# Optimization experiments

Hardware: AMD Instinct MI355X
Metric: run time of the kernel (lower is better)

The kernel has to match this reference:

```python
import jax, jax.numpy as jnp
import numpy as np


def setup_inputs() -> dict:
    key = jax.random.key(0)
    k1, k2, k3 = jax.random.split(key, 3)
    B, N, D = 4, 4096, 256
    val = jax.random.normal(k1, (B, N, D), dtype=jnp.float32)
    state = jax.random.normal(k2, (B, N), dtype=jnp.float32)
    # val projection weight, scaled for unit-variance outputs
    Wv = jax.random.normal(k3, (D, D), dtype=jnp.float32) / np.sqrt(D)
    return {"val": val, "state": state, "Wv": Wv}


def reference(val, state, Wv):
    # pairwise_fn: dot-product scores over all node pairs -> [B, N, N]
    scores = jnp.einsum("bnd,bmd->bnm", val, val)
    # edge_compress_fn: softsign (non-softmax elementwise nonlinearity)
    edges = scores / (1.0 + jnp.abs(scores))
    # state_proj_fn = identity, val_proj_fn = linear
    projected_state = state                                  # [B, N]
    projected_val = jnp.einsum("bmd,de->bme", val, Wv)       # [B, N, D]
    # dual aggregation reusing the same edge matrix
    delta_state = jnp.einsum("bnm,bm->bn", edges, projected_state)
    delta_val = jnp.einsum("bnm,bmd->bnd", edges, projected_val)
    return (delta_state, delta_val)
```

## Files before the change

### kernel.cpp

```cpp
#include <hip/hip_runtime.h>

typedef unsigned short u16;
typedef unsigned char u8;
typedef unsigned int u32;
typedef __bf16 bf16x8 __attribute__((ext_vector_type(8)));
typedef float  f32x16 __attribute__((ext_vector_type(16)));
typedef int    i32x4  __attribute__((ext_vector_type(4)));
typedef int    i32x16 __attribute__((ext_vector_type(16)));

#define NB 4
#define NN 4096
#define ND 256

#define QPV (127.0f / 4.5f)
#define DPV (4.5f / 16129.0f)
#define QST (127.0f / 4.6f)
#define DST (4.6f / 16129.0f)
#define MAGIC 12582912.0f

__device__ __forceinline__ u16 f2bf(float x) { return __builtin_bit_cast(u16, (__bf16)x); }
__device__ __forceinline__ u32 fbits(float x) { return __builtin_bit_cast(u32, x); }

__device__ __forceinline__ u32 packlow4(float a, float b, float c, float d) {
    u32 p = __builtin_amdgcn_perm(fbits(b), fbits(a), 0x00000400u);
    u32 q = __builtin_amdgcn_perm(fbits(d), fbits(c), 0x00000400u);
    return __builtin_amdgcn_perm(q, p, 0x05040100u);
}

typedef __attribute__((address_space(1))) const u32 gas_u32;
typedef __attribute__((address_space(3))) u32 las_u32;
__device__ __forceinline__ void async_ld16(void* lds, const void* g) {
    __builtin_amdgcn_global_load_lds((gas_u32*)g, (las_u32*)lds, 16, 0, 0);
}


__global__ __launch_bounds__(256) void k_prep(const float* __restrict__ val,
                                              const float* __restrict__ state,
                                              const float* __restrict__ Wv,
                                              u16* __restrict__ kq, u8* __restrict__ kq8,
                                              float* __restrict__ srow,
                                              u8* __restrict__ vp8, u16* __restrict__ wv) {
    int tid = threadIdx.x;
    int bid = blockIdx.x;
    if (bid < 512) {
        __shared__ float t[32 * 257];
        __shared__ float rmax[32];
        const float* src = val + (size_t)bid * 32 * 256;
        #pragma unroll
        for (int k = 0; k < 8; k++) {
            int idx = tid + k * 256;
            int row = idx >> 6, c4 = idx & 63;
            float4 v = *(const float4*)(src + row * 256 + c4 * 4);
            float* p = t + row * 257 + c4 * 4;
            p[0] = v.x; p[1] = v.y; p[2] = v.z; p[3] = v.w;
        }
        __syncthreads();
        {
            int row = tid >> 3, seg = tid & 7;
            float m = 0.0f;
            #pragma unroll
            for (int i = 0; i < 32; i++) m = fmaxf(m, fabsf(t[row * 257 + seg + i * 8]));
            m = fmaxf(m, __shfl_down(m, 4));
            m = fmaxf(m, __shfl_down(m, 2));
            m = fmaxf(m, __shfl_down(m, 1));
            if (seg == 0) {
                m = fmaxf(m, 1e-20f);
                rmax[row] = m;
                srow[bid * 32 + row] = m * (1.0f / 127.0f);
            }
        }
        __syncthreads();
        u16* dst = kq + (size_t)bid * 16 * 512;
        #pragma unroll
        for (int k = 0; k < 4; k++) {
            int flat = tid + k * 256;
            int s = flat >> 6, l = flat & 63;
            int l31 = l & 31, h = l >> 5;
            const float* p = t + l31 * 257 + s * 16 + h * 8;
            union { u16 o[8]; uint4 q; } u;
            #pragma unroll
            for (int j = 0; j < 8; j++) u.o[j] = f2bf(p[j]);
            *(uint4*)(dst + (size_t)flat * 8) = u.q;
        }
        u8* dst8 = kq8 + (size_t)bid * 8192;
        #pragma unroll
        for (int k = 0; k < 2; k++) {
            int flat = tid + k * 256;
            int s = flat >> 6, l = flat & 63;
            int l31 = l & 31, h = l >> 5;
            float r127 = 127.0f / rmax[l31];
            const float* p = t + l31 * 257 + s * 32 + h * 16;
            u32 d[4];
            #pragma unroll
            for (int g = 0; g < 4; g++)
                d[g] = packlow4(fmaf(p[4 * g + 0], r127, MAGIC), fmaf(p[4 * g + 1], r127, MAGIC),
                                fmaf(p[4 * g + 2], r127, MAGIC), fmaf(p[4 * g + 3], r127, MAGIC));
            *(uint4*)(dst8 + (size_t)flat * 16) = make_uint4(d[0], d[1], d[2], d[3]);
        }
    } else if (bid < 516) {
        int b = bid - 512;
        __shared__ u8 qs[4096];
        #pragma unroll
        for (int k = 0; k < 16; k++) {
            int i = tid + k * 256;
            float x = fminf(fmaxf(state[b * 4096 + i] * QST, -127.0f), 127.0f);
            qs[i] = (u8)(fbits(x + MAGIC) & 255);
        }
        __syncthreads();
        #pragma unroll
        for (int k = 0; k < 32; k++) {
            int chunk = tid + k * 256;
            int strip = chunk >> 6, lane = chunk & 63, h = (lane >> 5) & 1;
            i32x4 v = *(const i32x4*)(qs + strip * 32 + h * 16);
            *(i32x4*)(vp8 + ((size_t)((b * 128 + strip) * 9 + 8)) * 1024 + (chunk & 63) * 16) = v;
        }
    } else {
        __shared__ u16 t2[256 * 33];
        int es = bid - 516, e0 = es * 32;
        #pragma unroll
        for (int k = 0; k < 8; k++) {
            int idx = tid + k * 256;
            int row = idx >> 3, c4 = idx & 7;
            float4 v = *(const float4*)(Wv + row * 256 + e0 + c4 * 4);
            u16* p = t2 + row * 33 + c4 * 4;
            p[0] = f2bf(v.x); p[1] = f2bf(v.y); p[2] = f2bf(v.z); p[3] = f2bf(v.w);
        }
        __syncthreads();
        u16* dst = wv + (size_t)es * 16 * 512;
        #pragma unroll
        for (int k = 0; k < 4; k++) {
            int flat = tid + k * 256;
            int s = flat >> 6, l = flat & 63;
            int l31 = l & 31, h = l >> 5;
            union { u16 o[8]; uint4 q; } u;
            #pragma unroll
            for (int j = 0; j < 8; j++) u.o[j] = t2[(s * 16 + h * 8 + j) * 33 + l31];
            *(uint4*)(dst + (size_t)flat * 8) = u.q;
        }
    }
}

__global__ __launch_bounds__(256) void k_pv(const u16* __restrict__ kq, const u16* __restrict__ wv,
                                            u8* __restrict__ vp8) {
    __shared__ u8 tp[4][32 * 48];
    int tid = threadIdx.x;
    int w = tid >> 6, lane = tid & 63;
    int l31 = lane & 31, h = lane >> 5;
    int wid = blockIdx.x * 4 + w;
    int bb = wid >> 8, es = (wid >> 5) & 7, qb = wid & 31;
    const u16* wvb = wv + (size_t)(es * 16) * 512 + lane * 8;
    const u16* kqb = kq + ((size_t)(bb * 128 + qb * 4) * 16) * 512 + lane * 8;
    f32x16 acc[4] = {};
    for (int s = 0; s < 16; s++) {
        bf16x8 af = *(const bf16x8*)(wvb + s * 512);
        #pragma unroll
        for (int qt = 0; qt < 4; qt++) {
            bf16x8 bfr = *(const bf16x8*)(kqb + (size_t)(qt * 16 + s) * 512);
            acc[qt] = __builtin_amdgcn_mfma_f32_32x32x16_bf16(af, bfr, acc[qt], 0, 0, 0);
        }
    }
    u8* myp = tp[w];
    #pragma unroll
    for (int qt = 0; qt < 4; qt++) {
        #pragma unroll
        for (int r = 0; r < 16; r++) {
            int erow = (r & 3) + 8 * (r >> 2) + 4 * h;
            float x = fminf(fmaxf(acc[qt][r] * QPV, -127.0f), 127.0f);
            myp[erow * 48 + l31] = (u8)(fbits(x + MAGIC) & 255);
        }
        i32x4 v = *(const i32x4*)(myp + l31 * 48 + h * 16);
        *(i32x4*)(vp8 + ((size_t)((bb * 128 + qb * 4 + qt) * 9 + es)) * 1024 + lane * 16) = v;
    }
}

__device__ __forceinline__ void stage_wave(u8* dst, const u8* src, int lane) {
    #pragma unroll
    for (int k = 0; k < 9; k++) {
        int c = lane + k * 64;
        async_ld16(dst + (size_t)c * 16, src + (size_t)c * 16);
    }
}

__global__ __launch_bounds__(256, 2) void k_main(const u8* __restrict__ kq8,
                                                 const u8* __restrict__ vp8,
                                                 const float* __restrict__ srow,
                                                 float* __restrict__ ds_out,
                                                 float* __restrict__ dval_out) {
    __shared__ u8 stage[2][4][9216];
    __shared__ int dsqi[4][32];

    int tid = threadIdx.x;
    int mq = tid >> 6, lane = tid & 63;
    int l31 = lane & 31, h = lane >> 5;

    int id = blockIdx.x;
    int xcd = id & 7;
    int bb = xcd >> 1;
    int t7 = ((xcd & 1) << 6) | (id >> 3);
    int q0 = t7 * 32;
    size_t bbase = (size_t)bb * 128;

    i32x4 qf[8];
    {
        const u8* qsrc = kq8 + (bbase + t7) * 8192 + lane * 16;
        #pragma unroll
        for (int s = 0; s < 8; s++) qf[s] = *(const i32x4*)(qsrc + (size_t)s * 1024);
    }
    float srq = srow[bb * 4096 + q0 + l31];

    i32x16 oacc[8] = {};
    i32x16 dsa = {};

    stage_wave(stage[0][mq], vp8 + (bbase + mq) * 9216, lane);

    for (int mt = 0; mt < 32; mt++) {
        const u8* kb = kq8 + (bbase + mt * 4 + mq) * 8192 + lane * 16;
        i32x4 kf[8];
        #pragma unroll
        for (int s = 0; s < 8; s++) kf[s] = *(const i32x4*)(kb + (size_t)s * 1024);
        const float* srm = srow + bb * 4096 + mt * 128 + mq * 32;
        float4 sg[4];
        #pragma unroll
        for (int g = 0; g < 4; g++) sg[g] = *(const float4*)(srm + g * 8 + h * 4);
        if (mt + 1 < 32)
            stage_wave(stage[(mt + 1) & 1][mq], vp8 + (bbase + (mt + 1) * 4 + mq) * 9216, lane);

        i32x16 sacc = {};
        #pragma unroll
        for (int s = 0; s < 8; s++)
            sacc = __builtin_amdgcn_mfma_i32_32x32x32_i8(kf[s], qf[s], sacc, 0, 0, 0);

        float cf[16];
        #pragma unroll
        for (int r = 0; r < 16; r++) {
            float sm = ((const float*)&sg[r >> 2])[r & 3] * srq;
            float xs = (float)sacc[r] * sm;
            float p = xs * __builtin_amdgcn_rcpf(1.0f + fabsf(xs));
            cf[r] = fmaf(p, 127.0f, MAGIC);
        }
        u32 w0 = packlow4(cf[0], cf[1], cf[2], cf[3]);
        u32 w1 = packlow4(cf[4], cf[5], cf[6], cf[7]);
        u32 w2 = packlow4(cf[8], cf[9], cf[10], cf[11]);
        u32 w3 = packlow4(cf[12], cf[13], cf[14], cf[15]);
        u32 x0 = (u32)__shfl_xor((int)w0, 32);
        u32 x1 = (u32)__shfl_xor((int)w1, 32);
        u32 x2 = (u32)__shfl_xor((int)w2, 32);
        u32 x3 = (u32)__shfl_xor((int)w3, 32);
        union { u32 wd[4]; i32x4 v; } pu;
        if (h == 0) { pu.wd[0] = w0; pu.wd[1] = x0; pu.wd[2] = w1; pu.wd[3] = x1; }
        else        { pu.wd[0] = x2; pu.wd[1] = w2; pu.wd[2] = x3; pu.wd[3] = w3; }
        i32x4 pf = pu.v;

        const u8* vb = stage[mt & 1][mq];
        #pragma unroll
        for (int et = 0; et < 8; et++) {
            i32x4 vf = *(const i32x4*)(vb + et * 1024 + lane * 16);
            oacc[et] = __builtin_amdgcn_mfma_i32_32x32x32_i8(pf, vf, oacc[et], 0, 0, 0);
        }
        {
            i32x4 sf = *(const i32x4*)(vb + 8 * 1024 + lane * 16);
            dsa = __builtin_amdgcn_mfma_i32_32x32x32_i8(pf, sf, dsa, 0, 0, 0);
        }
    }

    __syncthreads();

    if (l31 == 0) {
        #pragma unroll
        for (int r = 0; r < 16; r++) dsqi[mq][(r & 3) + 8 * (r >> 2) + 4 * h] = dsa[r];
    }
    int* red = (int*)stage;
    if (mq == 3) {
        #pragma unroll
        for (int et = 0; et < 8; et++)
            #pragma unroll
            for (int r = 0; r < 16; r++) {
                int row = (r & 3) + 8 * (r >> 2) + 4 * h;
                red[row * 256 + et * 32 + l31] = oacc[et][r];
            }
    }
    __syncthreads();
    if (mq == 2) {
        #pragma unroll
        for (int et = 0; et < 8; et++)
            #pragma unroll
            for (int r = 0; r < 16; r++) {
                int row = (r & 3) + 8 * (r >> 2) + 4 * h;
                red[row * 256 + et * 32 + l31] += oacc[et][r];
            }
    }
    __syncthreads();
    if (mq == 1) {
        #pragma unroll
        for (int et = 0; et < 8; et++)
            #pragma unroll
            for (int r = 0; r < 16; r++) {
                int row = (r & 3) + 8 * (r >> 2) + 4 * h;
                red[row * 256 + et * 32 + l31] += oacc[et][r];
            }
    }
    __syncthreads();
    if (mq == 0) {
        #pragma unroll
        for (int et = 0; et < 8; et++)
            #pragma unroll
            for (int r = 0; r < 16; r++) {
                int row = (r & 3) + 8 * (r >> 2) + 4 * h;
                int sum = oacc[et][r] + red[row * 256 + et * 32 + l31];
                dval_out[((size_t)(bb * 4096 + q0 + row)) * 256 + et * 32 + l31] = (float)sum * DPV;
            }
        if (lane < 32) {
            int d = dsqi[0][lane] + dsqi[1][lane] + dsqi[2][lane] + dsqi[3][lane];
            ds_out[bb * 4096 + q0 + lane] = (float)d * DST;
        }
    }
}

extern "C" void kernel_launch(void* const* d_in, const int* in_sizes, int n_in,
                              void* d_out, int out_size, void* d_ws, size_t ws_size,
                              hipStream_t stream) {
    const float* val   = (const float*)d_in[0];
    const float* state = (const float*)d_in[1];
    const float* Wv    = (const float*)d_in[2];

    float* ds_out   = (float*)d_out;
    float* dval_out = ds_out + NB * NN;

    u8*  kq8 = (u8*)d_ws;
    u8*  vp8 = kq8 + (size_t)NB * NN * ND;
    u16* kq  = (u16*)(vp8 + (size_t)NB * 128 * 9216);
    u16* wv  = kq + (size_t)NB * NN * ND;
    float* srow = (float*)(wv + 8 * 16 * 512);

    k_prep<<<524, 256, 0, stream>>>(val, state, Wv, kq, kq8, srow, vp8, wv);
    k_pv<<<256, 256, 0, stream>>>(kq, wv, vp8);
    k_main<<<512, 256, 0, stream>>>(kq8, vp8, srow, ds_out, dval_out);
}
```

Before: 149.5 us.

## Fuse val quantization into projection kernel and widen main kernel to 64 rows

The bf16 staging buffer for val is removed. The new projection kernel reads fp32 val tiles into LDS once and produces the int8 keys, the row scales and the projected int8 values from that single tile. Only small Wv and state preprocessing stays in a separate tiny kernel. The main kernel now runs 512-thread blocks covering 64 query rows in two strips, so each block reuses every key/value tile across twice as many rows. It also drops the async LDS double-buffer staging of values and loads value fragments straight from global memory, which risks exposing load latency inside the MFMA loop.

New measurement: 155.2 us. 1.04x slower.

```diff
diff --git a/kernel.cpp b/kernel.cpp
--- a/kernel.cpp
+++ b/kernel.cpp
@@ -27,96 +27,15 @@
     return __builtin_amdgcn_perm(q, p, 0x05040100u);
 }
 
-typedef __attribute__((address_space(1))) const u32 gas_u32;
-typedef __attribute__((address_space(3))) u32 las_u32;
-__device__ __forceinline__ void async_ld16(void* lds, const void* g) {
-    __builtin_amdgcn_global_load_lds((gas_u32*)g, (las_u32*)lds, 16, 0, 0);
-}
-
-
-__global__ __launch_bounds__(256) void k_prep(const float* __restrict__ val,
+
+__global__ __launch_bounds__(256) void k_misc(const float* __restrict__ Wv,
                                               const float* __restrict__ state,
-                                              const float* __restrict__ Wv,
-                                              u16* __restrict__ kq, u8* __restrict__ kq8,
-                                              float* __restrict__ srow,
-                                              u8* __restrict__ vp8, u16* __restrict__ wv) {
+                                              u16* __restrict__ wv, u8* __restrict__ vp8) {
     int tid = threadIdx.x;
     int bid = blockIdx.x;
-    if (bid < 512) {
-        __shared__ float t[32 * 257];
-        __shared__ float rmax[32];
-        const float* src = val + (size_t)bid * 32 * 256;
-        #pragma unroll
-        for (int k = 0; k < 8; k++) {
-            int idx = tid + k * 256;
-            int row = idx >> 6, c4 = idx & 63;
-            float4 v = *(const float4*)(src + row * 256 + c4 * 4);
-            float* p = t + row * 257 + c4 * 4;
-            p[0] = v.x; p[1] = v.y; p[2] = v.z; p[3] = v.w;
-        }
-        __syncthreads();
-        {
-            int row = tid >> 3, seg = tid & 7;
-            float m = 0.0f;
-            #pragma unroll
-            for (int i = 0; i < 32; i++) m = fmaxf(m, fabsf(t[row * 257 + seg + i * 8]));
-            m = fmaxf(m, __shfl_down(m, 4));
-            m = fmaxf(m, __shfl_down(m, 2));
-            m = fmaxf(m, __shfl_down(m, 1));
-            if (seg == 0) {
-                m = fmaxf(m, 1e-20f);
-                rmax[row] = m;
-                srow[bid * 32 + row] = m * (1.0f / 127.0f);
-            }
-        }
-        __syncthreads();
-        u16* dst = kq + (size_t)bid * 16 * 512;
-        #pragma unroll
-        for (int k = 0; k < 4; k++) {
-            int flat = tid + k * 256;
-            int s = flat >> 6, l = flat & 63;
-            int l31 = l & 31, h = l >> 5;
-            const float* p = t + l31 * 257 + s * 16 + h * 8;
-            union { u16 o[8]; uint4 q; } u;
-            #pragma unroll
-            for (int j = 0; j < 8; j++) u.o[j] = f2bf(p[j]);
-            *(uint4*)(dst + (size_t)flat * 8) = u.q;
-        }
-        u8* dst8 = kq8 + (size_t)bid * 8192;
-        #pragma unroll
-        for (int k = 0; k < 2; k++) {
-            int flat = tid + k * 256;
-            int s = flat >> 6, l = flat & 63;
-            int l31 = l & 31, h = l >> 5;
-            float r127 = 127.0f / rmax[l31];
-            const float* p = t + l31 * 257 + s * 32 + h * 16;
-            u32 d[4];
-            #pragma unroll
-            for (int g = 0; g < 4; g++)
-                d[g] = packlow4(fmaf(p[4 * g + 0], r127, MAGIC), fmaf(p[4 * g + 1], r127, MAGIC),
-                                fmaf(p[4 * g + 2], r127, MAGIC), fmaf(p[4 * g + 3], r127, MAGIC));
-            *(uint4*)(dst8 + (size_t)flat * 16) = make_uint4(d[0], d[1], d[2], d[3]);
-        }
-    } else if (bid < 516) {
-        int b = bid - 512;
-        __shared__ u8 qs[4096];
-        #pragma unroll
-        for (int k = 0; k < 16; k++) {
-            int i = tid + k * 256;
-            float x = fminf(fmaxf(state[b * 4096 + i] * QST, -127.0f), 127.0f);
-            qs[i] = (u8)(fbits(x + MAGIC) & 255);
-        }
-        __syncthreads();
-        #pragma unroll
-        for (int k = 0; k < 32; k++) {
-            int chunk = tid + k * 256;
-            int strip = chunk >> 6, lane = chunk & 63, h = (lane >> 5) & 1;
-            i32x4 v = *(const i32x4*)(qs + strip * 32 + h * 16);
-            *(i32x4*)(vp8 + ((size_t)((b * 128 + strip) * 9 + 8)) * 1024 + (chunk & 63) * 16) = v;
-        }
-    } else {
+    if (bid < 8) {
         __shared__ u16 t2[256 * 33];
-        int es = bid - 516, e0 = es * 32;
+        int es = bid, e0 = es * 32;
         #pragma unroll
         for (int k = 0; k < 8; k++) {
             int idx = tid + k * 256;
@@ -137,84 +56,157 @@
             for (int j = 0; j < 8; j++) u.o[j] = t2[(s * 16 + h * 8 + j) * 33 + l31];
             *(uint4*)(dst + (size_t)flat * 8) = u.q;
         }
-    }
-}
-
-__global__ __launch_bounds__(256) void k_pv(const u16* __restrict__ kq, const u16* __restrict__ wv,
-                                            u8* __restrict__ vp8) {
+    } else {
+        int b = bid - 8;
+        __shared__ u8 qs[4096];
+        #pragma unroll
+        for (int k = 0; k < 16; k++) {
+            int i = tid + k * 256;
+            float x = fminf(fmaxf(state[b * 4096 + i] * QST, -127.0f), 127.0f);
+            qs[i] = (u8)(fbits(x + MAGIC) & 255);
+        }
+        __syncthreads();
+        #pragma unroll
+        for (int k = 0; k < 32; k++) {
+            int chunk = tid + k * 256;
+            int strip = chunk >> 6, lane = chunk & 63, h = (lane >> 5) & 1;
+            i32x4 v = *(const i32x4*)(qs + strip * 32 + h * 16);
+            *(i32x4*)(vp8 + ((size_t)((b * 128 + strip) * 9 + 8)) * 1024 + (chunk & 63) * 16) = v;
+        }
+    }
+}
+
+#define TFS 260
+__global__ __launch_bounds__(256) void k_pv2(const float* __restrict__ val,
+                                             const u16* __restrict__ wv,
+                                             u8* __restrict__ kq8, u8* __restrict__ vp8,
+                                             float* __restrict__ srow) {
+    __shared__ float tf[64 * TFS];
+    __shared__ float rmax[64];
     __shared__ u8 tp[4][32 * 48];
+
     int tid = threadIdx.x;
     int w = tid >> 6, lane = tid & 63;
     int l31 = lane & 31, h = lane >> 5;
-    int wid = blockIdx.x * 4 + w;
-    int bb = wid >> 8, es = (wid >> 5) & 7, qb = wid & 31;
-    const u16* wvb = wv + (size_t)(es * 16) * 512 + lane * 8;
-    const u16* kqb = kq + ((size_t)(bb * 128 + qb * 4) * 16) * 512 + lane * 8;
-    f32x16 acc[4] = {};
+    int bs = blockIdx.x;
+
+    const float* src = val + (size_t)bs * 64 * 256;
+    #pragma unroll
+    for (int k = 0; k < 16; k++) {
+        int idx = tid + k * 256;
+        int row = idx >> 6, c4 = idx & 63;
+        float4 v = *(const float4*)(src + row * 256 + c4 * 4);
+        *(float4*)(tf + row * TFS + c4 * 4) = v;
+    }
+    __syncthreads();
+
+    {
+        int row = tid >> 2, seg = tid & 3;
+        float m = 0.0f;
+        #pragma unroll
+        for (int i = 0; i < 16; i++) {
+            float4 v = *(const float4*)(tf + row * TFS + seg * 4 + i * 16);
+            m = fmaxf(fmaxf(fabsf(v.x), fabsf(v.y)), fmaxf(fmaxf(fabsf(v.z), fabsf(v.w)), m));
+        }
+        m = fmaxf(m, __shfl_xor(m, 1));
+        m = fmaxf(m, __shfl_xor(m, 2));
+        if (seg == 0) {
+            m = fmaxf(m, 1e-20f);
+            rmax[row] = m;
+            srow[bs * 64 + row] = m * (1.0f / 127.0f);
+        }
+    }
+    __syncthreads();
+
+    #pragma unroll
+    for (int k = 0; k < 4; k++) {
+        int flat = tid + k * 256;
+        int strip = flat >> 9, rest = flat & 511;
+        int s = rest >> 6, l = rest & 63;
+        int fl31 = l & 31, fh = l >> 5;
+        int row = strip * 32 + fl31;
+        float r127 = 127.0f / rmax[row];
+        const float* p = tf + row * TFS + s * 32 + fh * 16;
+        u32 d[4];
+        #pragma unroll
+        for (int g = 0; g < 4; g++)
+            d[g] = packlow4(fmaf(p[4 * g + 0], r127, MAGIC), fmaf(p[4 * g + 1], r127, MAGIC),
+                            fmaf(p[4 * g + 2], r127, MAGIC), fmaf(p[4 * g + 3], r127, MAGIC));
+        *(uint4*)(kq8 + ((size_t)(bs * 2 + strip)) * 8192 + (size_t)(s * 64 + l) * 16) =
+            make_uint4(d[0], d[1], d[2], d[3]);
+    }
+
+    f32x16 acc[2][2] = {};
     for (int s = 0; s < 16; s++) {
-        bf16x8 af = *(const bf16x8*)(wvb + s * 512);
-        #pragma unroll
-        for (int qt = 0; qt < 4; qt++) {
-            bf16x8 bfr = *(const bf16x8*)(kqb + (size_t)(qt * 16 + s) * 512);
-            acc[qt] = __builtin_amdgcn_mfma_f32_32x32x16_bf16(af, bfr, acc[qt], 0, 0, 0);
+        bf16x8 bq[2];
+        #pragma unroll
+        for (int qt = 0; qt < 2; qt++) {
+            const float* p = tf + (qt * 32 + l31) * TFS + s * 16 + h * 8;
+            union { __bf16 e[8]; bf16x8 v; } u;
+            #pragma unroll
+            for (int j = 0; j < 8; j++) u.e[j] = (__bf16)p[j];
+            bq[qt] = u.v;
+        }
+        #pragma unroll
+        for (int ei = 0; ei < 2; ei++) {
+            int es = w * 2 + ei;
+            bf16x8 af = *(const bf16x8*)(wv + (size_t)(es * 16 + s) * 512 + lane * 8);
+            acc[ei][0] = __builtin_amdgcn_mfma_f32_32x32x16_bf16(af, bq[0], acc[ei][0], 0, 0, 0);
+            acc[ei][1] = __builtin_amdgcn_mfma_f32_32x32x16_bf16(af, bq[1], acc[ei][1], 0, 0, 0);
         }
     }
     u8* myp = tp[w];
     #pragma unroll
-    for (int qt = 0; qt < 4; qt++) {
-        #pragma unroll
-        for (int r = 0; r < 16; r++) {
-            int erow = (r & 3) + 8 * (r >> 2) + 4 * h;
-            float x = fminf(fmaxf(acc[qt][r] * QPV, -127.0f), 127.0f);
-            myp[erow * 48 + l31] = (u8)(fbits(x + MAGIC) & 255);
-        }
-        i32x4 v = *(const i32x4*)(myp + l31 * 48 + h * 16);
-        *(i32x4*)(vp8 + ((size_t)((bb * 128 + qb * 4 + qt) * 9 + es)) * 1024 + lane * 16) = v;
-    }
-}
-
-__device__ __forceinline__ void stage_wave(u8* dst, const u8* src, int lane) {
-    #pragma unroll
-    for (int k = 0; k < 9; k++) {
-        int c = lane + k * 64;
-        async_ld16(dst + (size_t)c * 16, src + (size_t)c * 16);
-    }
-}
-
-__global__ __launch_bounds__(256, 2) void k_main(const u8* __restrict__ kq8,
+    for (int ei = 0; ei < 2; ei++) {
+        int es = w * 2 + ei;
+        #pragma unroll
+        for (int qt = 0; qt < 2; qt++) {
+            #pragma unroll
+            for (int r = 0; r < 16; r++) {
+                int erow = (r & 3) + 8 * (r >> 2) + 4 * h;
+                float x = fminf(fmaxf(acc[ei][qt][r] * QPV, -127.0f), 127.0f);
+                myp[erow * 48 + l31] = (u8)(fbits(x + MAGIC) & 255);
+            }
+            i32x4 v = *(const i32x4*)(myp + l31 * 48 + h * 16);
+            *(i32x4*)(vp8 + ((size_t)((bs * 2 + qt) * 9 + es)) * 1024 + lane * 16) = v;
+        }
+    }
+}
+
+__global__ __launch_bounds__(512, 2) void k_main(const u8* __restrict__ kq8,
                                                  const u8* __restrict__ vp8,
                                                  const float* __restrict__ srow,
                                                  float* __restrict__ ds_out,
                                                  float* __restrict__ dval_out) {
-    __shared__ u8 stage[2][4][9216];
-    __shared__ int dsqi[4][32];
+    __shared__ int red[2 * 8192];
+    __shared__ int dsqi[2][4][32];
 
     int tid = threadIdx.x;
-    int mq = tid >> 6, lane = tid & 63;
+    int w = tid >> 6, lane = tid & 63;
     int l31 = lane & 31, h = lane >> 5;
+    int strip = w & 1, mq = w >> 1;
 
     int id = blockIdx.x;
     int xcd = id & 7;
     int bb = xcd >> 1;
-    int t7 = ((xcd & 1) << 6) | (id >> 3);
-    int q0 = t7 * 32;
+    int t6 = ((xcd & 1) << 5) | (id >> 3);
+    int q0 = t6 * 64;
     size_t bbase = (size_t)bb * 128;
 
     i32x4 qf[8];
     {
-        const u8* qsrc = kq8 + (bbase + t7) * 8192 + lane * 16;
+        const u8* qsrc = kq8 + (bbase + t6 * 2 + strip) * 8192 + lane * 16;
         #pragma unroll
         for (int s = 0; s < 8; s++) qf[s] = *(const i32x4*)(qsrc + (size_t)s * 1024);
     }
-    float srq = srow[bb * 4096 + q0 + l31];
+    float srq = srow[bb * 4096 + q0 + strip * 32 + l31];
 
     i32x16 oacc[8] = {};
     i32x16 dsa = {};
 
-    stage_wave(stage[0][mq], vp8 + (bbase + mq) * 9216, lane);
-
     for (int mt = 0; mt < 32; mt++) {
         const u8* kb = kq8 + (bbase + mt * 4 + mq) * 8192 + lane * 16;
+        const u8* vbG = vp8 + (bbase + mt * 4 + mq) * 9216 + lane * 16;
         i32x4 kf[8];
         #pragma unroll
         for (int s = 0; s < 8; s++) kf[s] = *(const i32x4*)(kb + (size_t)s * 1024);
@@ -222,8 +214,6 @@
         float4 sg[4];
         #pragma unroll
         for (int g = 0; g < 4; g++) sg[g] = *(const float4*)(srm + g * 8 + h * 4);
-        if (mt + 1 < 32)
-            stage_wave(stage[(mt + 1) & 1][mq], vp8 + (bbase + (mt + 1) * 4 + mq) * 9216, lane);
 
         i32x16 sacc = {};
         #pragma unroll
@@ -251,32 +241,30 @@
         else        { pu.wd[0] = x2; pu.wd[1] = w2; pu.wd[2] = x3; pu.wd[3] = w3; }
         i32x4 pf = pu.v;
 
-        const u8* vb = stage[mt & 1][mq];
         #pragma unroll
         for (int et = 0; et < 8; et++) {
-            i32x4 vf = *(const i32x4*)(vb + et * 1024 + lane * 16);
+            i32x4 vf = *(const i32x4*)(vbG + (size_t)et * 1024);
             oacc[et] = __builtin_amdgcn_mfma_i32_32x32x32_i8(pf, vf, oacc[et], 0, 0, 0);
         }
         {
-            i32x4 sf = *(const i32x4*)(vb + 8 * 1024 + lane * 16);
+            i32x4 sf = *(const i32x4*)(vbG + (size_t)8 * 1024);
             dsa = __builtin_amdgcn_mfma_i32_32x32x32_i8(pf, sf, dsa, 0, 0, 0);
         }
     }
 
     __syncthreads();
-
     if (l31 == 0) {
         #pragma unroll
-        for (int r = 0; r < 16; r++) dsqi[mq][(r & 3) + 8 * (r >> 2) + 4 * h] = dsa[r];
-    }
-    int* red = (int*)stage;
+        for (int r = 0; r < 16; r++) dsqi[strip][mq][(r & 3) + 8 * (r >> 2) + 4 * h] = dsa[r];
+    }
+    int* rd = red + strip * 8192;
     if (mq == 3) {
         #pragma unroll
         for (int et = 0; et < 8; et++)
             #pragma unroll
             for (int r = 0; r < 16; r++) {
                 int row = (r & 3) + 8 * (r >> 2) + 4 * h;
-                red[row * 256 + et * 32 + l31] = oacc[et][r];
+                rd[row * 256 + et * 32 + l31] = oacc[et][r];
             }
     }
     __syncthreads();
@@ -286,7 +274,7 @@
             #pragma unroll
             for (int r = 0; r < 16; r++) {
                 int row = (r & 3) + 8 * (r >> 2) + 4 * h;
-                red[row * 256 + et * 32 + l31] += oacc[et][r];
+                rd[row * 256 + et * 32 + l31] += oacc[et][r];
             }
     }
     __syncthreads();
@@ -296,7 +284,7 @@
             #pragma unroll
             for (int r = 0; r < 16; r++) {
                 int row = (r & 3) + 8 * (r >> 2) + 4 * h;
-                red[row * 256 + et * 32 + l31] += oacc[et][r];
+                rd[row * 256 + et * 32 + l31] += oacc[et][r];
             }
     }
     __syncthreads();
@@ -306,12 +294,14 @@
             #pragma unroll
             for (int r = 0; r < 16; r++) {
                 int row = (r & 3) + 8 * (r >> 2) + 4 * h;
-                int sum = oacc[et][r] + red[row * 256 + et * 32 + l31];
-                dval_out[((size_t)(bb * 4096 + q0 + row)) * 256 + et * 32 + l31] = (float)sum * DPV;
+                int sum = oacc[et][r] + rd[row * 256 + et * 32 + l31];
+                dval_out[((size_t)(bb * 4096 + q0 + strip * 32 + row)) * 256 + et * 32 + l31] =
+                    (float)sum * DPV;
             }
         if (lane < 32) {
-            int d = dsqi[0][lane] + dsqi[1][lane] + dsqi[2][lane] + dsqi[3][lane];
-            ds_out[bb * 4096 + q0 + lane] = (float)d * DST;
+            int d = dsqi[strip][0][lane] + dsqi[strip][1][lane] +
+                    dsqi[strip][2][lane] + dsqi[strip][3][lane];
+            ds_out[bb * 4096 + q0 + strip * 32 + lane] = (float)d * DST;
         }
     }
 }
@@ -328,11 +318,10 @@
 
     u8*  kq8 = (u8*)d_ws;
     u8*  vp8 = kq8 + (size_t)NB * NN * ND;
-    u16* kq  = (u16*)(vp8 + (size_t)NB * 128 * 9216);
-    u16* wv  = kq + (size_t)NB * NN * ND;
+    u16* wv  = (u16*)(vp8 + (size_t)NB * 128 * 9216);
     float* srow = (float*)(wv + 8 * 16 * 512);
 
-    k_prep<<<524, 256, 0, stream>>>(val, state, Wv, kq, kq8, srow, vp8, wv);
-    k_pv<<<256, 256, 0, stream>>>(kq, wv, vp8);
-    k_main<<<512, 256, 0, stream>>>(kq8, vp8, srow, ds_out, dval_out);
-}
+    k_misc<<<12, 256, 0, stream>>>(Wv, state, wv, vp8);
+    k_pv2<<<256, 256, 0, stream>>>(val, wv, kq8, vp8, srow);
+    k_main<<<256, 512, 0, stream>>>(kq8, vp8, srow, ds_out, dval_out);
+}
```
